# Kernel tuning notes

Hardware: AMD Instinct MI355X
Metric: run time of the kernel (lower is better)

The kernel has to match this reference:

```python
import jax, jax.numpy as jnp
import numpy as np

B, F0, K = 256, 40, 32          # batch, num fields, embedding dim
CIN_SIZE = [200, 200]            # layer widths (field_num[1:])


def setup_inputs() -> dict:
    key = jax.random.key(0)
    ks = jax.random.split(key, 1 + 4 * len(CIN_SIZE))
    field_num = [F0] + CIN_SIZE
    d = {"inputs": jax.random.normal(ks[0], (B, F0, K), dtype=jnp.float32)}
    for i in range(len(CIN_SIZE)):
        # W_query: (1, Fi, K); W_key/W_value: (1, F0, K); cin_W: (1, F0*Fi, F_{i+1})
        d[f"wq{i}"] = jax.random.normal(ks[1 + 4 * i], (1, field_num[i], K), dtype=jnp.float32) * 0.05
        d[f"wk{i}"] = jax.random.normal(ks[2 + 4 * i], (1, F0, K), dtype=jnp.float32) * 0.05
        d[f"wv{i}"] = jax.random.normal(ks[3 + 4 * i], (1, F0, K), dtype=jnp.float32) * 0.05
        lim = (6.0 / (F0 * field_num[i] + field_num[i + 1])) ** 0.5  # glorot uniform
        d[f"cw{i}"] = jax.random.uniform(ks[4 + 4 * i], (1, F0 * field_num[i], field_num[i + 1]),
                                         minval=-lim, maxval=lim, dtype=jnp.float32)
    return d


def _cin(inputs, params):
    # inputs: [B, F0, K]; params: list of (wq, wk, wv, cw) per CIN layer
    Bb, F0_, Kk = inputs.shape
    res = inputs
    outs = []
    for (wq, wk, wv, cw) in params:
        x0_wk = inputs * wk                 # [B, F0, K]
        x0_wv = inputs * wv                 # [B, F0, K]
        xi_wq = res * wq                    # [B, Fi, K]
        # per-embedding-slot outer product scores: phi[b,k,f0,fi]
        phi = jnp.einsum('bfk,bgk->bkfg', x0_wk, xi_wq)
        # exp + normalize over F0 axis == softmax over axis=2
        alpha = jax.nn.softmax(phi, axis=2)                      # [B, K, F0, Fi]
        x = alpha * jnp.transpose(x0_wv, (0, 2, 1))[:, :, :, None]  # [B, K, F0, Fi]
        x = x.reshape(Bb, Kk, -1)           # flatten (f0, fi) row-major -> f0*Fi + fi
        # conv1d with kernel width 1 == channel matmul: [B, K, F0*Fi] @ [F0*Fi, F_{i+1}]
        out = jnp.einsum('bkc,cj->bjk', x, cw[0])                # [B, F_{i+1}, K]
        outs.append(out)
        res = out
    cat = jnp.concatenate(outs, axis=1)     # [B, sum(cin_size), K]
    return cat.sum(axis=-1)                 # [B, sum(cin_size)]


def reference(inputs, wq0, wk0, wv0, cw0, wq1, wk1, wv1, cw1):
    return _cin(inputs, [(wq0, wk0, wv0, cw0), (wq1, wk1, wv1, cw1)])
```

## Files before the change

### kernel.cpp

```cpp
#include <hip/hip_runtime.h>
#include <hip/hip_bf16.h>


#define NF0  40
#define KD   32
#define NJ   200
#define NTHR 512
#define G0   120
#define G1   600

typedef short bf16x8 __attribute__((ext_vector_type(8)));
typedef float f32x16 __attribute__((ext_vector_type(16)));
typedef unsigned short u16;
typedef unsigned int   u32;

static __device__ __forceinline__ u16 f2bf(float f) {
    __hip_bfloat16 h = __float2bfloat16(f);
    return *reinterpret_cast<u16*>(&h);
}

template<int FI>
__global__ __launch_bounds__(256)
void pack_b(const float* __restrict__ cw, u16* __restrict__ bp) {
    __shared__ u16 s[48][33];
    const int fi = blockIdx.x, nt = blockIdx.y;
    const int t = threadIdx.x;
    for (int idx = t; idx < 48 * 32; idx += 256) {
        int f0 = idx >> 5, jj = idx & 31, j = nt * 32 + jj;
        float v = (f0 < NF0 && j < NJ) ? cw[(size_t)(f0 * FI + fi) * NJ + j] : 0.f;
        s[f0][jj] = f2bf(v);
    }
    __syncthreads();
    if (t < 192) {
        const int g = t >> 6, l = t & 63;
        u16 v[8];
        #pragma unroll
        for (int i = 0; i < 8; ++i) v[i] = s[g * 16 + 8 * (l >> 5) + i][l & 31];
        constexpr int G = FI * 3;
        *reinterpret_cast<bf16x8*>(bp + ((size_t)(nt * G + fi * 3 + g) * 64 + l) * 8)
            = *reinterpret_cast<const bf16x8*>(v);
    }
}

__global__ __launch_bounds__(NTHR, 2)
void cin_fused(const float* __restrict__ x0,
               const float* __restrict__ wq0, const float* __restrict__ wk0,
               const float* __restrict__ wv0,
               const float* __restrict__ wq1, const float* __restrict__ wk1,
               const float* __restrict__ wv1,
               const u16* __restrict__ bp0, const u16* __restrict__ bp1,
               float* __restrict__ out) {
    __shared__ float s_res[NJ][33];
    __shared__ float s_o1[224];
    const int tid = threadIdx.x, b = blockIdx.x;
    const int wid = tid >> 6, lane = tid & 63;
    const int sk = lane & 31, sh = lane >> 5;
    const bool hb = (lane >= 32);

    for (int i = tid; i < NJ * 33; i += NTHR) (&s_res[0][0])[i] = 0.f;
    if (tid < 224) s_o1[tid] = 0.f;

    float xkr[24], xvr[24];
    f32x16 acc[7];

    auto load_xw = [&](const float* wk, const float* wv) {
        #pragma unroll
        for (int m = 0; m < 24; ++m) {
            const int f0 = sh * 24 + m;
            if (f0 < NF0) {
                const float v = x0[(size_t)b * 1280 + f0 * 32 + sk];
                xkr[m] = v * wk[f0 * 32 + sk];
                xvr[m] = v * wv[f0 * 32 + sk];
            } else { xkr[m] = 0.f; xvr[m] = 0.f; }
        }
    };
    auto zacc = [&]() {
        #pragma unroll
        for (int nt = 0; nt < 7; ++nt)
            #pragma unroll
            for (int r = 0; r < 16; ++r) acc[nt][r] = 0.f;
    };

    auto do_fi = [&](float q, const u16* __restrict__ bp, int G, int g0) {
        float e[24], d = 0.f;
        #pragma unroll
        for (int m = 0; m < 24; ++m) { e[m] = __expf(xkr[m] * q); d += e[m]; }
        if (sh) d -= 8.0f;
        d += __shfl_xor(d, 32);
        const float r = 1.0f / d;
        u32 pk[12];
        #pragma unroll
        for (int p = 0; p < 12; ++p)
            pk[p] = (u32)f2bf(e[2*p] * r * xvr[2*p])
                  | ((u32)f2bf(e[2*p+1] * r * xvr[2*p+1]) << 16);
        u32 tmp[4];
        #pragma unroll
        for (int j = 0; j < 4; ++j) tmp[j] = (u32)__shfl_xor((int)pk[4 + j], 32);
        #pragma unroll
        for (int s = 0; s < 3; ++s) {
            u32 a4[4];
            #pragma unroll
            for (int j = 0; j < 4; ++j)
                a4[j] = (s == 0) ? (hb ? tmp[j] : pk[j])
                      : (s == 1) ? (hb ? pk[j] : pk[8 + j])
                                 : (hb ? pk[8 + j] : tmp[j]);
            bf16x8 av;
            __builtin_memcpy(&av, a4, 16);
            const u16* bgp = bp + ((size_t)(g0 + s) * 64 + lane) * 8;
            #pragma unroll
            for (int nt = 0; nt < 7; ++nt) {
                bf16x8 bv = *reinterpret_cast<const bf16x8*>(bgp + (size_t)nt * G * 512);
                acc[nt] = __builtin_amdgcn_mfma_f32_32x32x16_bf16(av, bv, acc[nt], 0, 0, 0);
            }
        }
    };

    load_xw(wk0, wv0);
    zacc();
    for (int t = 0; t < 5; ++t) {
        const int fi = wid + t * 8;
        const float q = x0[(size_t)b * 1280 + fi * 32 + sk] * wq0[fi * 32 + sk];
        do_fi(q, bp0, G0, fi * 3);
    }
    __syncthreads();
    #pragma unroll
    for (int nt = 0; nt < 7; ++nt) {
        const int j = nt * 32 + sk;
        if (j < NJ) {
            #pragma unroll
            for (int r = 0; r < 16; ++r) {
                const int k = (r & 3) + 8 * (r >> 2) + 4 * sh;
                atomicAdd(&s_res[j][k], acc[nt][r]);
            }
        }
    }
    __syncthreads();

    if (tid < NJ) {
        float s = 0.f;
        #pragma unroll
        for (int k = 0; k < 32; ++k) s += s_res[tid][k];
        out[(size_t)b * 400 + tid] = s;
    }

    load_xw(wk1, wv1);
    zacc();
    for (int t = 0; t < 25; ++t) {
        const int fi = wid + t * 8;
        const float q = s_res[fi][sk] * wq1[fi * 32 + sk];
        do_fi(q, bp1, G1, fi * 3);
    }
    #pragma unroll
    for (int nt = 0; nt < 7; ++nt) {
        float s = 0.f;
        #pragma unroll
        for (int r = 0; r < 16; ++r) s += acc[nt][r];
        s += __shfl_xor(s, 32);
        const int j = nt * 32 + sk;
        if (!hb && j < NJ) atomicAdd(&s_o1[j], s);
    }
    __syncthreads();
    if (tid < NJ) out[(size_t)b * 400 + 200 + tid] = s_o1[tid];
}

extern "C" void kernel_launch(void* const* d_in, const int* in_sizes, int n_in,
                              void* d_out, int out_size, void* d_ws, size_t ws_size,
                              hipStream_t stream) {
    const float* x0  = (const float*)d_in[0];
    const float* wq0 = (const float*)d_in[1];
    const float* wk0 = (const float*)d_in[2];
    const float* wv0 = (const float*)d_in[3];
    const float* cw0 = (const float*)d_in[4];
    const float* wq1 = (const float*)d_in[5];
    const float* wk1 = (const float*)d_in[6];
    const float* wv1 = (const float*)d_in[7];
    const float* cw1 = (const float*)d_in[8];
    float* out = (float*)d_out;

    char* ws = (char*)d_ws;
    u16* bp0 = (u16*)ws;
    u16* bp1 = (u16*)(ws + 860160);

    pack_b<40> <<<dim3(40, 7),  256, 0, stream>>>(cw0, bp0);
    pack_b<200><<<dim3(200, 7), 256, 0, stream>>>(cw1, bp1);

    cin_fused<<<256, NTHR, 0, stream>>>(x0, wq0, wk0, wv0,
                                        wq1, wk1, wv1, bp0, bp1, out);
}
```

Baseline: 220.4 us.

## Split fused CIN kernel into per-layer kernels with shared-memory A tiles and split-K

Replaces the single per-batch fused kernel with two kernels. Layer 0 splits output columns across two blocks per batch and writes the intermediate result to global memory as bf16. Layer 1 pairs two batches per block so each B fragment feeds two MFMAs, and splits the Fi reduction four ways with atomic adds into a zeroed output. Softmax-weighted A tiles are staged through swizzled shared memory instead of per-lane registers and shuffles, which is meant to raise occupancy and grid parallelism beyond 256 blocks. The cost is an extra memset, a global round trip for the intermediate, bf16 rounding of the intermediate, and nondeterministic float atomics.

```diff
diff --git a/kernel.cpp b/kernel.cpp
--- a/kernel.cpp
+++ b/kernel.cpp
@@ -2,21 +2,24 @@
 #include <hip/hip_bf16.h>
 
 
-#define NF0  40
-#define KD   32
-#define NJ   200
-#define NTHR 512
-#define G0   120
-#define G1   600
+#define NF0 40
+#define NJ  200
 
 typedef short bf16x8 __attribute__((ext_vector_type(8)));
 typedef float f32x16 __attribute__((ext_vector_type(16)));
 typedef unsigned short u16;
 typedef unsigned int   u32;
+typedef unsigned long long u64;
 
 static __device__ __forceinline__ u16 f2bf(float f) {
     __hip_bfloat16 h = __float2bfloat16(f);
     return *reinterpret_cast<u16*>(&h);
+}
+static __device__ __forceinline__ float bf2f(u16 u) {
+    u32 x = ((u32)u) << 16;
+    float f;
+    __builtin_memcpy(&f, &x, 4);
+    return f;
 }
 
 template<int FI>
@@ -42,125 +45,213 @@
     }
 }
 
-__global__ __launch_bounds__(NTHR, 2)
-void cin_fused(const float* __restrict__ x0,
-               const float* __restrict__ wq0, const float* __restrict__ wk0,
-               const float* __restrict__ wv0,
-               const float* __restrict__ wq1, const float* __restrict__ wk1,
-               const float* __restrict__ wv1,
-               const u16* __restrict__ bp0, const u16* __restrict__ bp1,
-               float* __restrict__ out) {
-    __shared__ float s_res[NJ][33];
-    __shared__ float s_o1[224];
-    const int tid = threadIdx.x, b = blockIdx.x;
+__global__ __launch_bounds__(512, 6)
+void cin_l0(const float* __restrict__ x0,
+            const float* __restrict__ wq, const float* __restrict__ wk,
+            const float* __restrict__ wv,
+            const u16* __restrict__ bp,
+            u16* __restrict__ resh, float* __restrict__ out) {
+    __shared__ float s_xk[48 * 32], s_xv[48 * 32];
+    __shared__ char  s_XT[32 * 768];
+
+    const int tid = threadIdx.x;
+    const int b = blockIdx.x >> 1, jh = blockIdx.x & 1;
     const int wid = tid >> 6, lane = tid & 63;
-    const int sk = lane & 31, sh = lane >> 5;
-    const bool hb = (lane >= 32);
-
-    for (int i = tid; i < NJ * 33; i += NTHR) (&s_res[0][0])[i] = 0.f;
-    if (tid < 224) s_o1[tid] = 0.f;
-
-    float xkr[24], xvr[24];
-    f32x16 acc[7];
-
-    auto load_xw = [&](const float* wk, const float* wv) {
-        #pragma unroll
-        for (int m = 0; m < 24; ++m) {
-            const int f0 = sh * 24 + m;
-            if (f0 < NF0) {
-                const float v = x0[(size_t)b * 1280 + f0 * 32 + sk];
-                xkr[m] = v * wk[f0 * 32 + sk];
-                xvr[m] = v * wv[f0 * 32 + sk];
-            } else { xkr[m] = 0.f; xvr[m] = 0.f; }
-        }
-    };
-    auto zacc = [&]() {
-        #pragma unroll
-        for (int nt = 0; nt < 7; ++nt)
-            #pragma unroll
-            for (int r = 0; r < 16; ++r) acc[nt][r] = 0.f;
-    };
-
-    auto do_fi = [&](float q, const u16* __restrict__ bp, int G, int g0) {
-        float e[24], d = 0.f;
-        #pragma unroll
-        for (int m = 0; m < 24; ++m) { e[m] = __expf(xkr[m] * q); d += e[m]; }
-        if (sh) d -= 8.0f;
+    const int k = lane & 31, h = lane >> 5;
+
+    for (int i = tid; i < 32 * 768 / 8; i += 512) ((u64*)s_XT)[i] = 0ull;
+    for (int i = tid; i < 1536; i += 512) {
+        const int r = i >> 5, kk = i & 31;
+        float xk = 0.f, xv = 0.f;
+        if (r < NF0) {
+            const float v = x0[(size_t)b * 1280 + r * 32 + kk];
+            xk = v * wk[r * 32 + kk];
+            xv = v * wv[r * 32 + kk];
+        }
+        s_xk[i] = xk; s_xv[i] = xv;
+    }
+    __syncthreads();
+
+    const int sfil = wid;
+    const int soff = sfil * 96 + h * 40;
+    const int sswz = (k & 7) << 4;
+    char* srb = s_XT + k * 768;
+
+    const int nt = jh * 4 + wid;
+    const bool hasnt = jh ? (wid < 3) : (wid < 4);
+    const int arow = lane & 31;
+    char* apb = s_XT + arow * 768;
+    const int aswz = (arow & 7) << 4;
+    const int ah = h * 16;
+
+    float qx = x0[(size_t)b * 1280 + sfil * 32 + k];
+    float qw = wq[sfil * 32 + k];
+
+    f32x16 acc;
+    #pragma unroll
+    for (int r = 0; r < 16; ++r) acc[r] = 0.f;
+
+    for (int ch = 0; ch < 5; ++ch) {
+        const float q = qx * qw;
+        if (ch + 1 < 5) {
+            const int fi = (ch + 1) * 8 + sfil;
+            qx = x0[(size_t)b * 1280 + fi * 32 + k];
+            qw = wq[fi * 32 + k];
+        }
+        float d = 0.f;
+        const int fb = h * 20;
+        #pragma unroll
+        for (int i = 0; i < 20; ++i) d += __expf(s_xk[(fb + i) * 32 + k] * q);
         d += __shfl_xor(d, 32);
-        const float r = 1.0f / d;
-        u32 pk[12];
-        #pragma unroll
-        for (int p = 0; p < 12; ++p)
-            pk[p] = (u32)f2bf(e[2*p] * r * xvr[2*p])
-                  | ((u32)f2bf(e[2*p+1] * r * xvr[2*p+1]) << 16);
-        u32 tmp[4];
-        #pragma unroll
-        for (int j = 0; j < 4; ++j) tmp[j] = (u32)__shfl_xor((int)pk[4 + j], 32);
-        #pragma unroll
-        for (int s = 0; s < 3; ++s) {
-            u32 a4[4];
-            #pragma unroll
-            for (int j = 0; j < 4; ++j)
-                a4[j] = (s == 0) ? (hb ? tmp[j] : pk[j])
-                      : (s == 1) ? (hb ? pk[j] : pk[8 + j])
-                                 : (hb ? pk[8 + j] : tmp[j]);
-            bf16x8 av;
-            __builtin_memcpy(&av, a4, 16);
-            const u16* bgp = bp + ((size_t)(g0 + s) * 64 + lane) * 8;
-            #pragma unroll
-            for (int nt = 0; nt < 7; ++nt) {
-                bf16x8 bv = *reinterpret_cast<const bf16x8*>(bgp + (size_t)nt * G * 512);
-                acc[nt] = __builtin_amdgcn_mfma_f32_32x32x16_bf16(av, bv, acc[nt], 0, 0, 0);
+        const float rcp = 1.0f / d;
+        #pragma unroll
+        for (int p = 0; p < 10; ++p) {
+            const int f0 = fb + 2 * p;
+            const float y0 = __expf(s_xk[f0 * 32 + k] * q)       * rcp * s_xv[f0 * 32 + k];
+            const float y1 = __expf(s_xk[(f0 + 1) * 32 + k] * q) * rcp * s_xv[(f0 + 1) * 32 + k];
+            *reinterpret_cast<u32*>(srb + ((soff + p * 4) ^ sswz))
+                = (u32)f2bf(y0) | ((u32)f2bf(y1) << 16);
+        }
+        __syncthreads();
+        __builtin_amdgcn_s_setprio(1);
+        if (hasnt) {
+            #pragma unroll
+            for (int ks = 0; ks < 24; ++ks) {
+                bf16x8 bv = *reinterpret_cast<const bf16x8*>(
+                    bp + ((size_t)(nt * 120 + ch * 24 + ks) * 64 + lane) * 8);
+                bf16x8 av = *reinterpret_cast<const bf16x8*>(
+                    apb + ((ks * 32 + ah) ^ aswz));
+                acc = __builtin_amdgcn_mfma_f32_32x32x16_bf16(av, bv, acc, 0, 0, 0);
             }
         }
-    };
-
-    load_xw(wk0, wv0);
-    zacc();
-    for (int t = 0; t < 5; ++t) {
-        const int fi = wid + t * 8;
-        const float q = x0[(size_t)b * 1280 + fi * 32 + sk] * wq0[fi * 32 + sk];
-        do_fi(q, bp0, G0, fi * 3);
+        __builtin_amdgcn_s_setprio(0);
+        __syncthreads();
+    }
+
+    if (hasnt) {
+        const int j = nt * 32 + (lane & 31);
+        if (j < NJ) {
+            u16* dst = resh + (size_t)b * 6400 + j * 32;
+            #pragma unroll
+            for (int rg = 0; rg < 4; ++rg) {
+                u64 w = (u64)f2bf(acc[4*rg+0]) | ((u64)f2bf(acc[4*rg+1]) << 16)
+                      | ((u64)f2bf(acc[4*rg+2]) << 32) | ((u64)f2bf(acc[4*rg+3]) << 48);
+                *reinterpret_cast<u64*>(dst + 8 * rg + 4 * h) = w;
+            }
+            float s = 0.f;
+            #pragma unroll
+            for (int r = 0; r < 16; ++r) s += acc[r];
+            s += __shfl_xor(s, 32);
+            if (lane < 32) out[(size_t)b * 400 + j] = s;
+        }
+    }
+}
+
+__global__ __launch_bounds__(512, 6)
+void cin_l1(const float* __restrict__ x0, const u16* __restrict__ resh,
+            const float* __restrict__ wq, const float* __restrict__ wk,
+            const float* __restrict__ wv,
+            const u16* __restrict__ bp, float* __restrict__ out) {
+    __shared__ float s_xk[2 * 48 * 32], s_xv[2 * 48 * 32];
+    __shared__ char  s_XT[64 * 384];
+
+    const int tid = threadIdx.x;
+    const int bg = blockIdx.x >> 2, split = blockIdx.x & 3;
+    const int b0 = bg * 2;
+    const int fbase = split * 52;
+    const int nch = (split == 3) ? 11 : 13;
+    const int wid = tid >> 6, lane = tid & 63;
+    const int k = lane & 31, h = lane >> 5;
+
+    for (int i = tid; i < 64 * 384 / 8; i += 512) ((u64*)s_XT)[i] = 0ull;
+    for (int i = tid; i < 3072; i += 512) {
+        const int bb = i / 1536, rr = i - bb * 1536;
+        const int r = rr >> 5, kk = rr & 31;
+        float xk = 0.f, xv = 0.f;
+        if (r < NF0) {
+            const float v = x0[(size_t)(b0 + bb) * 1280 + r * 32 + kk];
+            xk = v * wk[r * 32 + kk];
+            xv = v * wv[r * 32 + kk];
+        }
+        s_xk[i] = xk; s_xv[i] = xv;
     }
     __syncthreads();
+
+    const int sbb = tid >> 8, sfil = (tid >> 6) & 3;
+    const int srow = sbb * 32 + k;
+    const int soff = sfil * 96 + h * 40;
+    const int sswz = (srow & 7) << 4;
+    char* srb = s_XT + srow * 384;
+    const float* xkp = s_xk + sbb * 1536;
+    const float* xvp = s_xv + sbb * 1536;
+
+    const int nt = wid;
+    const bool hasnt = (wid < 7);
+    const int arow = lane & 31;
+    const int ah = h * 16;
+
+    u16   qr = resh[(size_t)(b0 + sbb) * 6400 + (fbase + sfil) * 32 + k];
+    float qw = wq[(fbase + sfil) * 32 + k];
+
+    f32x16 acc0, acc1;
     #pragma unroll
-    for (int nt = 0; nt < 7; ++nt) {
-        const int j = nt * 32 + sk;
-        if (j < NJ) {
-            #pragma unroll
-            for (int r = 0; r < 16; ++r) {
-                const int k = (r & 3) + 8 * (r >> 2) + 4 * sh;
-                atomicAdd(&s_res[j][k], acc[nt][r]);
+    for (int r = 0; r < 16; ++r) { acc0[r] = 0.f; acc1[r] = 0.f; }
+
+    for (int ch = 0; ch < nch; ++ch) {
+        const float q = bf2f(qr) * qw;
+        if (ch + 1 < nch) {
+            const int fi = fbase + (ch + 1) * 4 + sfil;
+            qr = resh[(size_t)(b0 + sbb) * 6400 + fi * 32 + k];
+            qw = wq[fi * 32 + k];
+        }
+        float d = 0.f;
+        const int fb = h * 20;
+        #pragma unroll
+        for (int i = 0; i < 20; ++i) d += __expf(xkp[(fb + i) * 32 + k] * q);
+        d += __shfl_xor(d, 32);
+        const float rcp = 1.0f / d;
+        #pragma unroll
+        for (int p = 0; p < 10; ++p) {
+            const int f0 = fb + 2 * p;
+            const float y0 = __expf(xkp[f0 * 32 + k] * q)       * rcp * xvp[f0 * 32 + k];
+            const float y1 = __expf(xkp[(f0 + 1) * 32 + k] * q) * rcp * xvp[(f0 + 1) * 32 + k];
+            *reinterpret_cast<u32*>(srb + ((soff + p * 4) ^ sswz))
+                = (u32)f2bf(y0) | ((u32)f2bf(y1) << 16);
+        }
+        __syncthreads();
+        __builtin_amdgcn_s_setprio(1);
+        if (hasnt) {
+            const int gbase = fbase * 3 + ch * 12;
+            #pragma unroll
+            for (int ks = 0; ks < 12; ++ks) {
+                bf16x8 bv = *reinterpret_cast<const bf16x8*>(
+                    bp + ((size_t)(nt * 600 + gbase + ks) * 64 + lane) * 8);
+                const int cb = ks * 32 + ah;
+                bf16x8 a0 = *reinterpret_cast<const bf16x8*>(
+                    s_XT + arow * 384 + (cb ^ ((arow & 7) << 4)));
+                const int brow = 32 + arow;
+                bf16x8 a1 = *reinterpret_cast<const bf16x8*>(
+                    s_XT + brow * 384 + (cb ^ ((brow & 7) << 4)));
+                acc0 = __builtin_amdgcn_mfma_f32_32x32x16_bf16(a0, bv, acc0, 0, 0, 0);
+                acc1 = __builtin_amdgcn_mfma_f32_32x32x16_bf16(a1, bv, acc1, 0, 0, 0);
             }
         }
-    }
-    __syncthreads();
-
-    if (tid < NJ) {
-        float s = 0.f;
-        #pragma unroll
-        for (int k = 0; k < 32; ++k) s += s_res[tid][k];
-        out[(size_t)b * 400 + tid] = s;
-    }
-
-    load_xw(wk1, wv1);
-    zacc();
-    for (int t = 0; t < 25; ++t) {
-        const int fi = wid + t * 8;
-        const float q = s_res[fi][sk] * wq1[fi * 32 + sk];
-        do_fi(q, bp1, G1, fi * 3);
-    }
-    #pragma unroll
-    for (int nt = 0; nt < 7; ++nt) {
-        float s = 0.f;
-        #pragma unroll
-        for (int r = 0; r < 16; ++r) s += acc[nt][r];
-        s += __shfl_xor(s, 32);
-        const int j = nt * 32 + sk;
-        if (!hb && j < NJ) atomicAdd(&s_o1[j], s);
-    }
-    __syncthreads();
-    if (tid < NJ) out[(size_t)b * 400 + 200 + tid] = s_o1[tid];
+        __builtin_amdgcn_s_setprio(0);
+        __syncthreads();
+    }
+
+    if (hasnt) {
+        const int j = nt * 32 + (lane & 31);
+        float s0 = 0.f, s1 = 0.f;
+        #pragma unroll
+        for (int r = 0; r < 16; ++r) { s0 += acc0[r]; s1 += acc1[r]; }
+        s0 += __shfl_xor(s0, 32);
+        s1 += __shfl_xor(s1, 32);
+        if (lane < 32 && j < NJ) {
+            atomicAdd(&out[(size_t)b0 * 400 + 200 + j], s0);
+            atomicAdd(&out[(size_t)(b0 + 1) * 400 + 200 + j], s1);
+        }
+    }
 }
 
 extern "C" void kernel_launch(void* const* d_in, const int* in_sizes, int n_in,
@@ -178,12 +269,15 @@
     float* out = (float*)d_out;
 
     char* ws = (char*)d_ws;
-    u16* bp0 = (u16*)ws;
-    u16* bp1 = (u16*)(ws + 860160);
+    u16* resh = (u16*)ws;
+    u16* bp0  = (u16*)(ws + 3276800);
+    u16* bp1  = (u16*)(ws + 3276800 + 860160);
+
+    hipMemsetAsync(d_out, 0, (size_t)out_size * 4, stream);
 
     pack_b<40> <<<dim3(40, 7),  256, 0, stream>>>(cw0, bp0);
     pack_b<200><<<dim3(200, 7), 256, 0, stream>>>(cw1, bp1);
 
-    cin_fused<<<256, NTHR, 0, stream>>>(x0, wq0, wk0, wv0,
-                                        wq1, wk1, wv1, bp0, bp1, out);
-}
+    cin_l0<<<512, 512, 0, stream>>>(x0, wq0, wk0, wv0, bp0, resh, out);
+    cin_l1<<<512, 512, 0, stream>>>(x0, resh, wq1, wk1, wv1, bp1, out);
+}
```

Result: faster. 205.5 us (-6.8%).
